# Performance work log

Hardware: AMD Instinct MI355X
Metric: run time of the kernel (lower is better)

The kernel has to match this reference:

```python
import jax, jax.numpy as jnp
import numpy as np

SEQ_LS = [512, 512, 512, 512]
HEADS = 8
DIM_HEAD = 64
DIM = 512
INNER = HEADS * DIM_HEAD  # 512
N = sum(SEQ_LS)           # 2048
B = 4
EPS = 1e-5

# static modality id per token position: [N]
MOD_IDS = jnp.asarray(np.repeat(np.arange(len(SEQ_LS)), SEQ_LS))


def setup_inputs() -> dict:
    key = jax.random.key(0)
    ks = jax.random.split(key, 6)
    x = jax.random.normal(ks[0], (B, N, DIM), dtype=jnp.float32)
    m_labels = jnp.ones((B, len(SEQ_LS)), dtype=jnp.int64 if jax.config.jax_enable_x64 else jnp.int32)
    gamma = jnp.ones((DIM,), dtype=jnp.float32)
    beta = jnp.zeros((DIM,), dtype=jnp.float32)
    w_qkv = jax.random.normal(ks[1], (DIM, 3 * INNER), dtype=jnp.float32) * (DIM ** -0.5)
    w_out = jax.random.normal(ks[2], (INNER, DIM), dtype=jnp.float32) * (INNER ** -0.5)
    b_out = jnp.zeros((DIM,), dtype=jnp.float32)
    return {"x": x, "m_labels": m_labels, "gamma": gamma, "beta": beta,
            "w_qkv": w_qkv, "w_out": w_out, "b_out": b_out}


def _additive_mask(m_labels):
    # present[b, n] = modality of token n is present in sample b
    present = (m_labels[:, MOD_IDS] != 0)                       # [B, N] bool
    pair_ok = present[:, :, None] & present[:, None, :]         # [B, N, N]
    neg_inf = jnp.float32(-jnp.inf)
    return jnp.where(pair_ok, jnp.float32(0.0), neg_inf)        # [B, N, N]


def reference(x, m_labels, gamma, beta, w_qkv, w_out, b_out):
    # LayerNorm(dim)
    mu = jnp.mean(x, axis=-1, keepdims=True)
    var = jnp.mean(jnp.square(x - mu), axis=-1, keepdims=True)
    xn = (x - mu) * jax.lax.rsqrt(var + EPS) * gamma + beta

    # QKV projection (no bias), split heads
    qkv = jnp.einsum('bnd,de->bne', xn, w_qkv)                  # [B, N, 3*INNER]
    q, k, v = jnp.split(qkv, 3, axis=-1)
    def heads(t):
        return t.reshape(B, N, HEADS, DIM_HEAD).transpose(0, 2, 1, 3)  # [B, H, N, Dh]
    q, k, v = heads(q), heads(k), heads(v)

    scale = DIM_HEAD ** -0.5
    dots = jnp.einsum('bhnd,bhmd->bhnm', q, k) * scale          # [B, H, N, N]
    dots = dots + _additive_mask(m_labels)[:, None, :, :]
    attn = jax.nn.softmax(dots, axis=-1)
    out = jnp.einsum('bhnm,bhmd->bhnd', attn, v)                # [B, H, N, Dh]
    out = out.transpose(0, 2, 1, 3).reshape(B, N, INNER)        # [B, N, INNER]
    return jnp.einsum('bni,io->bno', out, w_out) + b_out        # [B, N, DIM]
```

## Files before the change

### kernel.cpp

```cpp
#include <hip/hip_runtime.h>

#define DIMD 512
#define NTOK 2048
#define HEADS 8
#define DH 64

typedef __attribute__((ext_vector_type(4))) float f32x4;
typedef __attribute__((ext_vector_type(8))) __bf16 bf16x8;

#define MFMA16(a, b, c) __builtin_amdgcn_mfma_f32_16x16x32_bf16((a), (b), (c), 0, 0, 0)

__device__ __forceinline__ unsigned short f2bf(float f) {
  unsigned int u = __float_as_uint(f);
  u += 0x7fffu + ((u >> 16) & 1u);
  return (unsigned short)(u >> 16);
}

__device__ __forceinline__ void gl2lds16(const void* g, void* l) {
  auto gp = reinterpret_cast<__attribute__((address_space(1))) unsigned int*>(
      reinterpret_cast<unsigned long long>(g));
  auto lp = reinterpret_cast<__attribute__((address_space(3))) unsigned int*>(
      reinterpret_cast<unsigned long long>(l));
  __builtin_amdgcn_global_load_lds(gp, lp, 16, 0, 0);
}

__global__ __launch_bounds__(256) void ln_kernel(const float* __restrict__ x,
                                                 const float* __restrict__ gamma,
                                                 const float* __restrict__ beta,
                                                 unsigned short* __restrict__ xn) {
  const int row = blockIdx.x * 4 + (threadIdx.x >> 6);
  const int lane = threadIdx.x & 63;
  const float4* xr = (const float4*)(x + (size_t)row * DIMD);
  float4 a = xr[lane];
  float4 b = xr[lane + 64];
  float s = a.x + a.y + a.z + a.w + b.x + b.y + b.z + b.w;
  for (int off = 1; off < 64; off <<= 1) s += __shfl_xor(s, off, 64);
  float mu = s * (1.0f / DIMD);
  float d0 = a.x - mu, d1 = a.y - mu, d2 = a.z - mu, d3 = a.w - mu;
  float e0 = b.x - mu, e1 = b.y - mu, e2 = b.z - mu, e3 = b.w - mu;
  float v = d0 * d0 + d1 * d1 + d2 * d2 + d3 * d3 + e0 * e0 + e1 * e1 + e2 * e2 + e3 * e3;
  for (int off = 1; off < 64; off <<= 1) v += __shfl_xor(v, off, 64);
  float rs = rsqrtf(v * (1.0f / DIMD) + 1e-5f);
  const float4* g4 = (const float4*)gamma;
  const float4* be4 = (const float4*)beta;
  float4 ga = g4[lane], gb = g4[lane + 64];
  float4 ba = be4[lane], bb = be4[lane + 64];
  unsigned int p0 = (unsigned)f2bf(d0 * rs * ga.x + ba.x) | ((unsigned)f2bf(d1 * rs * ga.y + ba.y) << 16);
  unsigned int p1 = (unsigned)f2bf(d2 * rs * ga.z + ba.z) | ((unsigned)f2bf(d3 * rs * ga.w + ba.w) << 16);
  unsigned int p2 = (unsigned)f2bf(e0 * rs * gb.x + bb.x) | ((unsigned)f2bf(e1 * rs * gb.y + bb.y) << 16);
  unsigned int p3 = (unsigned)f2bf(e2 * rs * gb.z + bb.z) | ((unsigned)f2bf(e3 * rs * gb.w + bb.w) << 16);
  uint2 w0; w0.x = p0; w0.y = p1;
  uint2 w1; w1.x = p2; w1.y = p3;
  *(uint2*)&xn[(size_t)row * DIMD + lane * 4] = w0;
  *(uint2*)&xn[(size_t)row * DIMD + 256 + lane * 4] = w1;
}

__global__ __launch_bounds__(256) void wt_kernel(const float* __restrict__ w,
                                                 unsigned short* __restrict__ wt,
                                                 int R, int C) {
  __shared__ float t[32][33];
  int tx = threadIdx.x & 31, ty = threadIdx.x >> 5;
  int c0 = blockIdx.x * 32, r0 = blockIdx.y * 32;
  for (int i = 0; i < 4; i++)
    t[ty + 8 * i][tx] = w[(size_t)(r0 + ty + 8 * i) * C + c0 + tx];
  __syncthreads();
  for (int i = 0; i < 4; i++)
    wt[(size_t)(c0 + ty + 8 * i) * R + r0 + tx] = f2bf(t[tx][ty + 8 * i]);
}

__global__ __launch_bounds__(256, 2) void qkv_gemm(const unsigned short* __restrict__ A,
                                                   const unsigned short* __restrict__ Bt,
                                                   unsigned short* __restrict__ qb,
                                                   unsigned short* __restrict__ kb,
                                                   unsigned short* __restrict__ vtb) {
  __shared__ unsigned short As[2][128 * 64];
  __shared__ unsigned short Bs[2][128 * 64];
  const int tid = threadIdx.x;
  const int wave = tid >> 6, lane = tid & 63;
  const int row16 = lane & 15, quad = lane >> 4;
  const int rho = row16 & 7;
  const int m0 = blockIdx.x * 128;
  const int n0 = blockIdx.y * 128;
  const int rw = (wave & 1) * 64, cw = (wave >> 1) * 64;

  const char* Ab = (const char*)A;
  const char* Bb = (const char*)Bt;
#pragma unroll
  for (int i = 0; i < 4; i++) {
    int idx = i * 256 + tid;
    int r = idx >> 3;
    int c = (idx & 7) ^ (r & 7);
    gl2lds16(Ab + ((size_t)(m0 + r) * DIMD) * 2 + c * 16, (char*)As[0] + idx * 16);
    gl2lds16(Bb + ((size_t)(n0 + r) * DIMD) * 2 + c * 16, (char*)Bs[0] + idx * 16);
  }
  __syncthreads();

  f32x4 acc[4][4] = {};
  for (int kt = 0; kt < 8; kt++) {
    const int buf = kt & 1;
    if (kt < 7) {
      const int k0 = (kt + 1) * 64;
#pragma unroll
      for (int i = 0; i < 4; i++) {
        int idx = i * 256 + tid;
        int r = idx >> 3;
        int c = (idx & 7) ^ (r & 7);
        gl2lds16(Ab + ((size_t)(m0 + r) * DIMD + k0) * 2 + c * 16, (char*)As[buf ^ 1] + idx * 16);
        gl2lds16(Bb + ((size_t)(n0 + r) * DIMD + k0) * 2 + c * 16, (char*)Bs[buf ^ 1] + idx * 16);
      }
    }
#pragma unroll
    for (int ks = 0; ks < 2; ks++) {
      bf16x8 av[4], bv[4];
#pragma unroll
      for (int i = 0; i < 4; i++) {
        int Ra = rw + i * 16 + row16;
        int Rb = cw + i * 16 + row16;
        av[i] = *(const bf16x8*)&As[buf][Ra * 64 + (((ks * 4 + quad) ^ rho) * 8)];
        bv[i] = *(const bf16x8*)&Bs[buf][Rb * 64 + (((ks * 4 + quad) ^ rho) * 8)];
      }
#pragma unroll
      for (int i = 0; i < 4; i++)
#pragma unroll
        for (int j = 0; j < 4; j++) acc[i][j] = MFMA16(av[i], bv[j], acc[i][j]);
    }
    __syncthreads();
  }

  unsigned short* Ct = (unsigned short*)As;
#pragma unroll
  for (int i = 0; i < 4; i++)
#pragma unroll
    for (int j = 0; j < 4; j++)
#pragma unroll
      for (int r = 0; r < 4; r++)
        Ct[(rw + i * 16 + quad * 4 + r) * 136 + cw + j * 16 + row16] = f2bf(acc[i][j][r]);
  __syncthreads();

  const int sect = n0 >> 9;
  const int h0 = (n0 & 511) >> 6;
  const int b = m0 >> 11;
  const int nbase = m0 & 2047;
  if (sect < 2) {
    unsigned short* dst = (sect == 0) ? qb : kb;
#pragma unroll
    for (int i = 0; i < 8; i++) {
      int cid = i * 256 + tid;
      int row = cid >> 4, col0 = (cid & 15) * 8;
      int h = h0 + (col0 >> 6), d0 = col0 & 63;
      uint4 val = *(const uint4*)&Ct[row * 136 + col0];
      *(uint4*)&dst[(((size_t)(b * HEADS + h) * NTOK) + nbase + row) * DH + d0] = val;
    }
  } else {
#pragma unroll
    for (int u = 0; u < 4; u++) {
      int uid = u * 256 + tid;
      int col = uid >> 3, rc = (uid & 7) * 16;
      int h = h0 + (col >> 6), d = col & 63;
      unsigned short tmp[16];
#pragma unroll
      for (int j = 0; j < 16; j++) tmp[j] = Ct[(rc + j) * 136 + col];
      size_t base = ((size_t)(b * HEADS + h) * DH + d) * NTOK + nbase + rc;
      *(uint4*)&vtb[base] = *(uint4*)&tmp[0];
      *(uint4*)&vtb[base + 8] = *(uint4*)&tmp[8];
    }
  }
}

__global__ __launch_bounds__(256, 2) void attn_kernel(const unsigned short* __restrict__ qb,
                                                      const unsigned short* __restrict__ kb,
                                                      const unsigned short* __restrict__ vtb,
                                                      const int* __restrict__ mlab,
                                                      unsigned short* __restrict__ ao) {
  __shared__ unsigned short Ps[2][128 * 64];
  __shared__ unsigned short Ks[2][64 * 64];
  __shared__ unsigned short Vs[2][64 * 64];
  const int tid = threadIdx.x;
  const int wave = tid >> 6, lane = tid & 63;
  const int row16 = lane & 15, quad = lane >> 4;
  const int rho = row16 & 7;
  const int bh = blockIdx.y;
  const int b = bh >> 3, h = bh & 7;
  const int q0 = blockIdx.x * 128;

  const char* qg = (const char*)(qb + ((size_t)bh * NTOK + q0) * DH);
  const char* kgb = (const char*)(kb + (size_t)bh * NTOK * DH);
  const char* vgb = (const char*)(vtb + (size_t)bh * DH * NTOK);
  const int sr = tid >> 3;
  const int sc = (tid & 7) ^ (sr & 7);

#pragma unroll
  for (int i = 0; i < 4; i++)
    gl2lds16(qg + (sr + 32 * i) * 128 + sc * 16, (char*)Ps[0] + tid * 16 + i * 4096);
  gl2lds16(kgb + sr * 128 + sc * 16, (char*)Ks[0] + tid * 16);
  gl2lds16(kgb + (sr + 32) * 128 + sc * 16, (char*)Ks[0] + tid * 16 + 4096);
  gl2lds16(vgb + (size_t)sr * 4096 + sc * 16, (char*)Vs[0] + tid * 16);
  gl2lds16(vgb + (size_t)(sr + 32) * 4096 + sc * 16, (char*)Vs[0] + tid * 16 + 4096);
  __syncthreads();

  bf16x8 aq[2][2];
#pragma unroll
  for (int qs = 0; qs < 2; qs++) {
    const int qrow = wave * 32 + qs * 16 + row16;
#pragma unroll
    for (int ki = 0; ki < 2; ki++)
      aq[qs][ki] = *(const bf16x8*)&Ps[0][qrow * 64 + (((ki * 4 + quad) ^ rho) * 8)];
  }
  __syncthreads();

  f32x4 accO[2][4] = {};
  float lsum[2][4] = {};
  const float cs = 0.125f * 1.44269504088896f;
  const float c0 = mlab[b * 4 + 0] ? -16.f : -100000.f;
  const float c1 = mlab[b * 4 + 1] ? -16.f : -100000.f;
  const float c2 = mlab[b * 4 + 2] ? -16.f : -100000.f;
  const float c3 = mlab[b * 4 + 3] ? -16.f : -100000.f;

  for (int t = 0; t < 32; t++) {
    const int buf = t & 1;
    if (t < 31) {
      const char* kg = kgb + (size_t)(t + 1) * 8192;
      char* lk = (char*)Ks[buf ^ 1];
      gl2lds16(kg + sr * 128 + sc * 16, lk + tid * 16);
      gl2lds16(kg + (sr + 32) * 128 + sc * 16, lk + tid * 16 + 4096);
    }
    f32x4 S[2][4];
#pragma unroll
    for (int f = 0; f < 4; f++) {
      const unsigned short* Kr = &Ks[buf][(f * 16 + row16) * 64];
      bf16x8 bk0 = *(const bf16x8*)&Kr[(quad ^ rho) * 8];
      bf16x8 bk1 = *(const bf16x8*)&Kr[((quad + 4) ^ rho) * 8];
#pragma unroll
      for (int qs = 0; qs < 2; qs++) {
        f32x4 z = {};
        z = MFMA16(aq[qs][0], bk0, z);
        z = MFMA16(aq[qs][1], bk1, z);
        S[qs][f] = z;
      }
    }
    const int mi = t >> 3;
    const float c = (mi == 0) ? c0 : (mi == 1) ? c1 : (mi == 2) ? c2 : c3;
    const int chbase = (row16 >> 3);
#pragma unroll
    for (int qs = 0; qs < 2; qs++)
#pragma unroll
      for (int f = 0; f < 4; f++) {
#pragma unroll
        for (int r = 0; r < 4; r++) {
          float p = exp2f(fmaf(S[qs][f][r], cs, c));
          lsum[qs][r] += p;
          const int prow = wave * 32 + qs * 16 + quad * 4 + r;
          Ps[buf][prow * 64 + ((((2 * f + chbase) ^ (prow & 7)) * 8) + (row16 & 7))] =
              (unsigned short)(__float_as_uint(p) >> 16);
        }
      }
    __syncthreads();
    if (t < 31) {
      const char* vg = vgb + (size_t)(t + 1) * 128;
      char* lv = (char*)Vs[buf ^ 1];
      gl2lds16(vg + (size_t)sr * 4096 + sc * 16, lv + tid * 16);
      gl2lds16(vg + (size_t)(sr + 32) * 4096 + sc * 16, lv + tid * 16 + 4096);
    }
    bf16x8 ap[2][2];
#pragma unroll
    for (int qs = 0; qs < 2; qs++) {
      const int qrow = wave * 32 + qs * 16 + row16;
#pragma unroll
      for (int ki = 0; ki < 2; ki++)
        ap[qs][ki] = *(const bf16x8*)&Ps[buf][qrow * 64 + (((ki * 4 + quad) ^ rho) * 8)];
    }
#pragma unroll
    for (int f = 0; f < 4; f++) {
      const unsigned short* Vr = &Vs[buf][(f * 16 + row16) * 64];
      bf16x8 bv0 = *(const bf16x8*)&Vr[(quad ^ rho) * 8];
      bf16x8 bv1 = *(const bf16x8*)&Vr[((quad + 4) ^ rho) * 8];
#pragma unroll
      for (int qs = 0; qs < 2; qs++) {
        accO[qs][f] = MFMA16(ap[qs][0], bv0, accO[qs][f]);
        accO[qs][f] = MFMA16(ap[qs][1], bv1, accO[qs][f]);
      }
    }
  }

#pragma unroll
  for (int qs = 0; qs < 2; qs++)
#pragma unroll
    for (int r = 0; r < 4; r++) {
      float s = lsum[qs][r];
      s += __shfl_xor(s, 1, 64);
      s += __shfl_xor(s, 2, 64);
      s += __shfl_xor(s, 4, 64);
      s += __shfl_xor(s, 8, 64);
      lsum[qs][r] = 1.0f / s;
    }
#pragma unroll
  for (int qs = 0; qs < 2; qs++)
#pragma unroll
    for (int f = 0; f < 4; f++)
#pragma unroll
      for (int r = 0; r < 4; r++) {
        int qr = q0 + wave * 32 + qs * 16 + quad * 4 + r;
        ao[((size_t)b * NTOK + qr) * DIMD + h * DH + f * 16 + row16] =
            f2bf(accO[qs][f][r] * lsum[qs][r]);
      }
}

__global__ __launch_bounds__(256, 2) void out_gemm(const unsigned short* __restrict__ A,
                                                   const unsigned short* __restrict__ Bt,
                                                   const float* __restrict__ bias,
                                                   float* __restrict__ out) {
  __shared__ unsigned short As[2][128 * 64];
  __shared__ unsigned short Bs[2][128 * 64];
  const int tid = threadIdx.x;
  const int wave = tid >> 6, lane = tid & 63;
  const int row16 = lane & 15, quad = lane >> 4;
  const int rho = row16 & 7;
  const int m0 = blockIdx.x * 128;
  const int n0 = blockIdx.y * 128;
  const int rw = (wave & 1) * 64, cw = (wave >> 1) * 64;

  const char* Ab = (const char*)A;
  const char* Bb = (const char*)Bt;
#pragma unroll
  for (int i = 0; i < 4; i++) {
    int idx = i * 256 + tid;
    int r = idx >> 3;
    int c = (idx & 7) ^ (r & 7);
    gl2lds16(Ab + ((size_t)(m0 + r) * DIMD) * 2 + c * 16, (char*)As[0] + idx * 16);
    gl2lds16(Bb + ((size_t)(n0 + r) * DIMD) * 2 + c * 16, (char*)Bs[0] + idx * 16);
  }
  __syncthreads();

  f32x4 acc[4][4] = {};
  for (int kt = 0; kt < 8; kt++) {
    const int buf = kt & 1;
    if (kt < 7) {
      const int k0 = (kt + 1) * 64;
#pragma unroll
      for (int i = 0; i < 4; i++) {
        int idx = i * 256 + tid;
        int r = idx >> 3;
        int c = (idx & 7) ^ (r & 7);
        gl2lds16(Ab + ((size_t)(m0 + r) * DIMD + k0) * 2 + c * 16, (char*)As[buf ^ 1] + idx * 16);
        gl2lds16(Bb + ((size_t)(n0 + r) * DIMD + k0) * 2 + c * 16, (char*)Bs[buf ^ 1] + idx * 16);
      }
    }
#pragma unroll
    for (int ks = 0; ks < 2; ks++) {
      bf16x8 av[4], bv[4];
#pragma unroll
      for (int i = 0; i < 4; i++) {
        int Ra = rw + i * 16 + row16;
        int Rb = cw + i * 16 + row16;
        av[i] = *(const bf16x8*)&As[buf][Ra * 64 + (((ks * 4 + quad) ^ rho) * 8)];
        bv[i] = *(const bf16x8*)&Bs[buf][Rb * 64 + (((ks * 4 + quad) ^ rho) * 8)];
      }
#pragma unroll
      for (int i = 0; i < 4; i++)
#pragma unroll
        for (int j = 0; j < 4; j++) acc[i][j] = MFMA16(av[i], bv[j], acc[i][j]);
    }
    __syncthreads();
  }

#pragma unroll
  for (int j = 0; j < 4; j++) {
    const int col = n0 + cw + j * 16 + row16;
    const float bv = bias[col];
#pragma unroll
    for (int i = 0; i < 4; i++)
#pragma unroll
      for (int r = 0; r < 4; r++) {
        const int row = m0 + rw + i * 16 + quad * 4 + r;
        out[(size_t)row * DIMD + col] = acc[i][j][r] + bv;
      }
  }
}

extern "C" void kernel_launch(void* const* d_in, const int* in_sizes, int n_in,
                              void* d_out, int out_size, void* d_ws, size_t ws_size,
                              hipStream_t stream) {
  const float* x = (const float*)d_in[0];
  const int* mlab = (const int*)d_in[1];
  const float* gamma = (const float*)d_in[2];
  const float* beta = (const float*)d_in[3];
  const float* w_qkv = (const float*)d_in[4];
  const float* w_out = (const float*)d_in[5];
  const float* b_out = (const float*)d_in[6];
  float* out = (float*)d_out;

  char* ws = (char*)d_ws;
  unsigned short* xn = (unsigned short*)(ws);
  unsigned short* wqkvT = (unsigned short*)(ws + 8388608);
  unsigned short* woutT = (unsigned short*)(ws + 9961472);
  unsigned short* qbuf = (unsigned short*)(ws + 10485760);
  unsigned short* kbuf = (unsigned short*)(ws + 18874368);
  unsigned short* vtbuf = (unsigned short*)(ws + 27262976);
  unsigned short* aobuf = (unsigned short*)(ws + 35651584);

  ln_kernel<<<2048, 256, 0, stream>>>(x, gamma, beta, xn);
  wt_kernel<<<dim3(48, 16), 256, 0, stream>>>(w_qkv, wqkvT, 512, 1536);
  wt_kernel<<<dim3(16, 16), 256, 0, stream>>>(w_out, woutT, 512, 512);
  qkv_gemm<<<dim3(64, 12), 256, 0, stream>>>(xn, wqkvT, qbuf, kbuf, vtbuf);
  attn_kernel<<<dim3(16, 32), 256, 0, stream>>>(qbuf, kbuf, vtbuf, mlab, aobuf);
  out_gemm<<<dim3(64, 4), 256, 0, stream>>>(aobuf, woutT, b_out, out);
}
```

Measured before the change: 186.5 us.

## Keep softmax probabilities in registers via transposed S and 16x16x16 MFMA for PV

The attention kernel now computes the transposed score tile (K as the A operand, Q as B), so each lane's probabilities line up with the B operand layout of the 16x16x16 bf16 MFMA. P is packed directly into registers instead of being written to and read back from LDS, which removes the P LDS round-trip and one barrier per iteration. The PV product accumulates a transposed output. V prefetch moves up beside the K prefetch, and the row-sum reduction uses cross-quad shuffles. In exchange it issues twice as many smaller MFMAs for PV, adds more V LDS reads of 8 bytes each, and frees 16 KB of LDS.

```diff
diff --git a/kernel.cpp b/kernel.cpp
--- a/kernel.cpp
+++ b/kernel.cpp
@@ -7,13 +7,19 @@
 
 typedef __attribute__((ext_vector_type(4))) float f32x4;
 typedef __attribute__((ext_vector_type(8))) __bf16 bf16x8;
+typedef __attribute__((ext_vector_type(4))) short s16x4;
 
 #define MFMA16(a, b, c) __builtin_amdgcn_mfma_f32_16x16x32_bf16((a), (b), (c), 0, 0, 0)
+#define MFMAK16(a, b, c) __builtin_amdgcn_mfma_f32_16x16x16bf16_1k((a), (b), (c), 0, 0, 0)
 
 __device__ __forceinline__ unsigned short f2bf(float f) {
   unsigned int u = __float_as_uint(f);
   u += 0x7fffu + ((u >> 16) & 1u);
   return (unsigned short)(u >> 16);
+}
+
+__device__ __forceinline__ unsigned packhi(float b, float a) {
+  return (__float_as_uint(b) >> 16) | (__float_as_uint(a) & 0xffff0000u);
 }
 
 __device__ __forceinline__ void gl2lds16(const void* g, void* l) {
@@ -172,7 +178,7 @@
                                                       const unsigned short* __restrict__ vtb,
                                                       const int* __restrict__ mlab,
                                                       unsigned short* __restrict__ ao) {
-  __shared__ unsigned short Ps[2][128 * 64];
+  __shared__ unsigned short Qs[128 * 64];
   __shared__ unsigned short Ks[2][64 * 64];
   __shared__ unsigned short Vs[2][64 * 64];
   const int tid = threadIdx.x;
@@ -191,7 +197,7 @@
 
 #pragma unroll
   for (int i = 0; i < 4; i++)
-    gl2lds16(qg + (sr + 32 * i) * 128 + sc * 16, (char*)Ps[0] + tid * 16 + i * 4096);
+    gl2lds16(qg + (sr + 32 * i) * 128 + sc * 16, (char*)Qs + tid * 16 + i * 4096);
   gl2lds16(kgb + sr * 128 + sc * 16, (char*)Ks[0] + tid * 16);
   gl2lds16(kgb + (sr + 32) * 128 + sc * 16, (char*)Ks[0] + tid * 16 + 4096);
   gl2lds16(vgb + (size_t)sr * 4096 + sc * 16, (char*)Vs[0] + tid * 16);
@@ -204,12 +210,11 @@
     const int qrow = wave * 32 + qs * 16 + row16;
 #pragma unroll
     for (int ki = 0; ki < 2; ki++)
-      aq[qs][ki] = *(const bf16x8*)&Ps[0][qrow * 64 + (((ki * 4 + quad) ^ rho) * 8)];
-  }
-  __syncthreads();
-
-  f32x4 accO[2][4] = {};
-  float lsum[2][4] = {};
+      aq[qs][ki] = *(const bf16x8*)&Qs[qrow * 64 + (((ki * 4 + quad) ^ rho) * 8)];
+  }
+
+  f32x4 accT[4][2] = {};
+  float lsum[2] = {0.f, 0.f};
   const float cs = 0.125f * 1.44269504088896f;
   const float c0 = mlab[b * 4 + 0] ? -16.f : -100000.f;
   const float c1 = mlab[b * 4 + 1] ? -16.f : -100000.f;
@@ -223,86 +228,72 @@
       char* lk = (char*)Ks[buf ^ 1];
       gl2lds16(kg + sr * 128 + sc * 16, lk + tid * 16);
       gl2lds16(kg + (sr + 32) * 128 + sc * 16, lk + tid * 16 + 4096);
-    }
-    f32x4 S[2][4];
-#pragma unroll
-    for (int f = 0; f < 4; f++) {
-      const unsigned short* Kr = &Ks[buf][(f * 16 + row16) * 64];
-      bf16x8 bk0 = *(const bf16x8*)&Kr[(quad ^ rho) * 8];
-      bf16x8 bk1 = *(const bf16x8*)&Kr[((quad + 4) ^ rho) * 8];
-#pragma unroll
-      for (int qs = 0; qs < 2; qs++) {
-        f32x4 z = {};
-        z = MFMA16(aq[qs][0], bk0, z);
-        z = MFMA16(aq[qs][1], bk1, z);
-        S[qs][f] = z;
-      }
-    }
-    const int mi = t >> 3;
-    const float c = (mi == 0) ? c0 : (mi == 1) ? c1 : (mi == 2) ? c2 : c3;
-    const int chbase = (row16 >> 3);
-#pragma unroll
-    for (int qs = 0; qs < 2; qs++)
-#pragma unroll
-      for (int f = 0; f < 4; f++) {
-#pragma unroll
-        for (int r = 0; r < 4; r++) {
-          float p = exp2f(fmaf(S[qs][f][r], cs, c));
-          lsum[qs][r] += p;
-          const int prow = wave * 32 + qs * 16 + quad * 4 + r;
-          Ps[buf][prow * 64 + ((((2 * f + chbase) ^ (prow & 7)) * 8) + (row16 & 7))] =
-              (unsigned short)(__float_as_uint(p) >> 16);
-        }
-      }
-    __syncthreads();
-    if (t < 31) {
       const char* vg = vgb + (size_t)(t + 1) * 128;
       char* lv = (char*)Vs[buf ^ 1];
       gl2lds16(vg + (size_t)sr * 4096 + sc * 16, lv + tid * 16);
       gl2lds16(vg + (size_t)(sr + 32) * 4096 + sc * 16, lv + tid * 16 + 4096);
     }
-    bf16x8 ap[2][2];
-#pragma unroll
-    for (int qs = 0; qs < 2; qs++) {
-      const int qrow = wave * 32 + qs * 16 + row16;
-#pragma unroll
-      for (int ki = 0; ki < 2; ki++)
-        ap[qs][ki] = *(const bf16x8*)&Ps[buf][qrow * 64 + (((ki * 4 + quad) ^ rho) * 8)];
-    }
+    f32x4 S[2][4];
 #pragma unroll
     for (int f = 0; f < 4; f++) {
-      const unsigned short* Vr = &Vs[buf][(f * 16 + row16) * 64];
-      bf16x8 bv0 = *(const bf16x8*)&Vr[(quad ^ rho) * 8];
-      bf16x8 bv1 = *(const bf16x8*)&Vr[((quad + 4) ^ rho) * 8];
+      const unsigned short* Kr = &Ks[buf][(f * 16 + row16) * 64];
+      bf16x8 ak0 = *(const bf16x8*)&Kr[(quad ^ rho) * 8];
+      bf16x8 ak1 = *(const bf16x8*)&Kr[((quad + 4) ^ rho) * 8];
 #pragma unroll
       for (int qs = 0; qs < 2; qs++) {
-        accO[qs][f] = MFMA16(ap[qs][0], bv0, accO[qs][f]);
-        accO[qs][f] = MFMA16(ap[qs][1], bv1, accO[qs][f]);
-      }
-    }
-  }
-
-#pragma unroll
-  for (int qs = 0; qs < 2; qs++)
-#pragma unroll
-    for (int r = 0; r < 4; r++) {
-      float s = lsum[qs][r];
-      s += __shfl_xor(s, 1, 64);
-      s += __shfl_xor(s, 2, 64);
-      s += __shfl_xor(s, 4, 64);
-      s += __shfl_xor(s, 8, 64);
-      lsum[qs][r] = 1.0f / s;
-    }
-#pragma unroll
-  for (int qs = 0; qs < 2; qs++)
-#pragma unroll
-    for (int f = 0; f < 4; f++)
-#pragma unroll
-      for (int r = 0; r < 4; r++) {
-        int qr = q0 + wave * 32 + qs * 16 + quad * 4 + r;
-        ao[((size_t)b * NTOK + qr) * DIMD + h * DH + f * 16 + row16] =
-            f2bf(accO[qs][f][r] * lsum[qs][r]);
-      }
+        f32x4 z = {};
+        z = MFMA16(ak0, aq[qs][0], z);
+        z = MFMA16(ak1, aq[qs][1], z);
+        S[qs][f] = z;
+      }
+    }
+    const int mi = t >> 3;
+    const float c = (mi == 0) ? c0 : (mi == 1) ? c1 : (mi == 2) ? c2 : c3;
+    s16x4 pf[2][4];
+#pragma unroll
+    for (int qs = 0; qs < 2; qs++)
+#pragma unroll
+      for (int f = 0; f < 4; f++) {
+        float p0 = exp2f(fmaf(S[qs][f][0], cs, c));
+        float p1 = exp2f(fmaf(S[qs][f][1], cs, c));
+        float p2 = exp2f(fmaf(S[qs][f][2], cs, c));
+        float p3 = exp2f(fmaf(S[qs][f][3], cs, c));
+        lsum[qs] += (p0 + p1) + (p2 + p3);
+        uint2 pk;
+        pk.x = packhi(p0, p1);
+        pk.y = packhi(p2, p3);
+        pf[qs][f] = *(s16x4*)&pk;
+      }
+#pragma unroll
+    for (int g = 0; g < 4; g++) {
+      const unsigned short* Vr = &Vs[buf][(g * 16 + row16) * 64];
+#pragma unroll
+      for (int u = 0; u < 4; u++) {
+        s16x4 va = *(const s16x4*)&Vr[(((2 * u + (quad >> 1)) ^ rho) * 8) + (quad & 1) * 4];
+#pragma unroll
+        for (int qs = 0; qs < 2; qs++) accT[g][qs] = MFMAK16(va, pf[qs][u], accT[g][qs]);
+      }
+    }
+    __syncthreads();
+  }
+
+#pragma unroll
+  for (int qs = 0; qs < 2; qs++) {
+    float s = lsum[qs];
+    s += __shfl_xor(s, 16, 64);
+    s += __shfl_xor(s, 32, 64);
+    lsum[qs] = 1.0f / s;
+  }
+#pragma unroll
+  for (int qs = 0; qs < 2; qs++) {
+    const int q = q0 + wave * 32 + qs * 16 + row16;
+    unsigned short* aor = ao + ((size_t)b * NTOK + q) * DIMD + h * DH;
+#pragma unroll
+    for (int g = 0; g < 4; g++)
+#pragma unroll
+      for (int r = 0; r < 4; r++)
+        aor[g * 16 + quad * 4 + r] = f2bf(accT[g][qs][r] * lsum[qs]);
+  }
 }
 
 __global__ __launch_bounds__(256, 2) void out_gemm(const unsigned short* __restrict__ A,
```

Result: faster. 178.4 us (-4.3%).
